# Kernel optimization log

Measured on AMD Instinct MI355X. Metric: run time of the kernel, lower is better.

The kernel has to match this reference:

```python
import jax, jax.numpy as jnp
import numpy as np

C = 64  # chunk size (hardcoded in DeltaCorrection.forward)


def setup_inputs() -> dict:
    key = jax.random.key(0)
    ks = jax.random.split(key, 6)
    B, H, N, d = 4, 16, 4096, 64
    q = jax.random.normal(ks[0], (B, H, N, d), jnp.float32)
    k = jax.random.normal(ks[1], (B, H, N, d), jnp.float32)
    v = jax.random.normal(ks[2], (B, H, N, d), jnp.float32)
    # gate projections: Linear(d, 1). Use small random weights so gates vary per token.
    w_decay = jax.random.normal(ks[3], (d, 1), jnp.float32) * 0.1
    b_decay = jnp.full((1,), -2.0, jnp.float32)
    w_write = jax.random.normal(ks[4], (d, 1), jnp.float32) * 0.1
    b_write = jnp.full((1,), -1.0, jnp.float32)
    out_scale = jnp.full((1,), 0.01, jnp.float32)
    return {"q": q, "k": k, "v": v, "w_decay": w_decay, "b_decay": b_decay,
            "w_write": w_write, "b_write": b_write, "out_scale": out_scale}


def _delta_correction(q, k, v, w_decay, b_decay, w_write, b_write, out_scale):
    B, H, N, d = q.shape
    assert N % C == 0  # pad branch is a no-op for our shapes
    beta = jax.nn.sigmoid(k @ w_write + b_write)   # (B,H,N,1) write strength
    alpha = jax.nn.sigmoid(k @ w_decay + b_decay)  # (B,H,N,1) decay
    k_norm = k / jnp.maximum(jnp.linalg.norm(k, axis=-1, keepdims=True), 1e-12)

    n_chunks = N // C
    q_c = q.reshape(B, H, n_chunks, C, d)
    k_c = k_norm.reshape(B, H, n_chunks, C, d)
    v_c = v.reshape(B, H, n_chunks, C, d)
    b_c = beta.reshape(B, H, n_chunks, C, 1)
    a_c = alpha.reshape(B, H, n_chunks, C, 1)

    # intra-chunk causal linear attention, scaled by per-key beta
    scores = jnp.einsum('bhnid,bhnjd->bhnij', q_c, k_c)      # (B,H,n,C,C)
    causal = jnp.tril(jnp.ones((C, C), q.dtype))
    scores = scores * causal * jnp.swapaxes(b_c, -1, -2)
    intra = jnp.einsum('bhnij,bhnjd->bhnid', scores, v_c)     # (B,H,n,C,d)

    # inter-chunk: sequential (d,d) state propagation via scan
    chunk_decay = jnp.mean(a_c, axis=3) ** C                  # (B,H,n,1)
    kv_all = jnp.einsum('bhnci,bhncj->bhnij', b_c * v_c, k_c) # (B,H,n,d,d)

    def step(S, inp):
        qc, kvc, dec = inp  # (B,H,C,d), (B,H,d,d), (B,H,1)
        inter = jnp.einsum('bhij,bhcj->bhci', S, qc)
        S = dec[..., None] * S + kvc
        return S, inter

    xs = (jnp.moveaxis(q_c, 2, 0), jnp.moveaxis(kv_all, 2, 0),
          jnp.moveaxis(chunk_decay, 2, 0))
    S0 = jnp.zeros((B, H, d, d), q.dtype)
    _, inter = jax.lax.scan(step, S0, xs)                     # (n,B,H,C,d)
    inter = jnp.moveaxis(inter, 0, 2)                         # (B,H,n,C,d)

    corrections = (intra + inter).reshape(B, H, N, d)
    return corrections * out_scale[0]


def reference(q, k, v, w_decay, b_decay, w_write, b_write, out_scale):
    return _delta_correction(q, k, v, w_decay, b_decay, w_write, b_write, out_scale)
```

## Files before the change

kernel.cpp:

```cpp
#include <hip/hip_runtime.h>
#include <math.h>


#define NCH 64
#define NBH 64

typedef __attribute__((ext_vector_type(8))) short bf16x8;
typedef __attribute__((ext_vector_type(4))) float f32x4;
typedef unsigned short ushort_t;

#define MFMA(a, b, c) __builtin_amdgcn_mfma_f32_16x16x32_bf16(a, b, c, 0, 0, 0)

__device__ __forceinline__ float sigf(float x) { return 1.0f / (1.0f + expf(-x)); }

__device__ __forceinline__ int swb(int row, int col) {
  return ((row << 7) + (col << 1)) ^ ((row & 7) << 4);
}

__device__ __forceinline__ void split1(float x, ushort_t& h, ushort_t& l) {
  unsigned xb = __float_as_uint(x);
  h = (ushort_t)(xb >> 16);
  float hf = __uint_as_float(xb & 0xFFFF0000u);
  float lf = x - hf;
  l = (ushort_t)(__float_as_uint(lf) >> 16);
}

__device__ __forceinline__ void st_split4(char* bh, char* bl, int row, int col, float4 v) {
  ushort_t h0, h1, h2, h3, l0, l1, l2, l3;
  split1(v.x, h0, l0); split1(v.y, h1, l1); split1(v.z, h2, l2); split1(v.w, h3, l3);
  uint2 hp, lp;
  hp.x = (unsigned)h0 | ((unsigned)h1 << 16); hp.y = (unsigned)h2 | ((unsigned)h3 << 16);
  lp.x = (unsigned)l0 | ((unsigned)l1 << 16); lp.y = (unsigned)l2 | ((unsigned)l3 << 16);
  int o = swb(row, col);
  *(uint2*)(bh + o) = hp;
  *(uint2*)(bl + o) = lp;
}

__device__ __forceinline__ bf16x8 ldfrag(const char* base, int mrow, int kk, int lane) {
  int r = mrow + (lane & 15);
  int c = kk + ((lane >> 4) << 3);
  return *(const bf16x8*)(base + swb(r, c));
}

__global__ __launch_bounds__(256) void k1_kvdecay(
    const float* __restrict__ kg, const float* __restrict__ vg,
    const float* __restrict__ w_decay, const float* __restrict__ b_decay,
    const float* __restrict__ w_write, const float* __restrict__ b_write,
    float* __restrict__ ws_kv, float* __restrict__ ws_decay) {
  __shared__ uint4 smraw[3072];
  __shared__ float abuf[64];
  char* sm = (char*)smraw;
  char* KT_H = sm;
  char* KT_L = sm + 8192;
  char* VT_H = sm + 16384;
  char* VT_L = sm + 24576;
  float* obuf = (float*)(sm + 32768);

  const int tid = threadIdx.x;
  const int lane = tid & 63, wv = tid >> 6;
  const int bh = blockIdx.x >> 6, cid = blockIdx.x & 63;
  const size_t gbase = (size_t)(bh * 4096 + cid * 64) * 64;

  {
    const int t = tid >> 2, g = tid & 3;
    const float* kp = kg + gbase + t * 64 + g * 16;
    const float* vp = vg + gbase + t * 64 + g * 16;
    float4 kr[4], vr[4];
#pragma unroll
    for (int u = 0; u < 4; ++u) { kr[u] = *(const float4*)(kp + 4 * u); vr[u] = *(const float4*)(vp + 4 * u); }
    float n2 = 0.f, dw = 0.f, da = 0.f;
#pragma unroll
    for (int u = 0; u < 4; ++u) {
      const float* wwp = w_write + g * 16 + 4 * u;
      const float* wdp = w_decay + g * 16 + 4 * u;
      float4 k4 = kr[u];
      n2 = fmaf(k4.x, k4.x, fmaf(k4.y, k4.y, fmaf(k4.z, k4.z, fmaf(k4.w, k4.w, n2))));
      dw = fmaf(k4.x, wwp[0], fmaf(k4.y, wwp[1], fmaf(k4.z, wwp[2], fmaf(k4.w, wwp[3], dw))));
      da = fmaf(k4.x, wdp[0], fmaf(k4.y, wdp[1], fmaf(k4.z, wdp[2], fmaf(k4.w, wdp[3], da))));
    }
    n2 += __shfl_xor(n2, 1, 64); n2 += __shfl_xor(n2, 2, 64);
    dw += __shfl_xor(dw, 1, 64); dw += __shfl_xor(dw, 2, 64);
    da += __shfl_xor(da, 1, 64); da += __shfl_xor(da, 2, 64);
    float beta  = sigf(dw + b_write[0]);
    float alpha = sigf(da + b_decay[0]);
    float fold  = beta / fmaxf(sqrtf(n2), 1e-12f);
    if (g == 0) abuf[t] = alpha;
#pragma unroll
    for (int u = 0; u < 4; ++u) {
      float kf[4] = {kr[u].x * fold, kr[u].y * fold, kr[u].z * fold, kr[u].w * fold};
      float vf[4] = {vr[u].x, vr[u].y, vr[u].z, vr[u].w};
#pragma unroll
      for (int e = 0; e < 4; ++e) {
        int row = g * 16 + 4 * u + e;
        ushort_t h, l;
        int o = swb(row, t);
        split1(kf[e], h, l);
        *(ushort_t*)(KT_H + o) = h; *(ushort_t*)(KT_L + o) = l;
        split1(vf[e], h, l);
        *(ushort_t*)(VT_H + o) = h; *(ushort_t*)(VT_L + o) = l;
      }
    }
  }
  __syncthreads();

  if (tid < 64) {
    float a = abuf[tid];
    for (int off = 32; off; off >>= 1) a += __shfl_down(a, off, 64);
    if (tid == 0) {
      float m = a * (1.0f / 64.0f);
      float p = m * m; p = p * p; p = p * p; p = p * p; p = p * p; p = p * p;
      ws_decay[bh * NCH + cid] = p;
    }
  }

  f32x4 z = {0.f, 0.f, 0.f, 0.f};
  f32x4 acc[4] = {z, z, z, z};
#pragma unroll
  for (int kk = 0; kk < 64; kk += 32) {
    bf16x8 ah = ldfrag(VT_H, wv * 16, kk, lane);
    bf16x8 al = ldfrag(VT_L, wv * 16, kk, lane);
#pragma unroll
    for (int jb = 0; jb < 4; ++jb) {
      bf16x8 bh_ = ldfrag(KT_H, jb * 16, kk, lane);
      bf16x8 bl_ = ldfrag(KT_L, jb * 16, kk, lane);
      acc[jb] = MFMA(ah, bh_, acc[jb]);
      acc[jb] = MFMA(ah, bl_, acc[jb]);
      acc[jb] = MFMA(al, bh_, acc[jb]);
    }
  }
#pragma unroll
  for (int jb = 0; jb < 4; ++jb) {
    int j = jb * 16 + (lane & 15);
    int i0 = wv * 16 + ((lane >> 4) << 2);
#pragma unroll
    for (int r = 0; r < 4; ++r) obuf[(i0 + r) * 64 + j] = acc[jb][r];
  }
  __syncthreads();
  float* kvout = ws_kv + (size_t)(bh * NCH + cid) * 4096;
#pragma unroll
  for (int rr = 0; rr < 4; ++rr) {
    int f = tid + 256 * rr;
    *(float4*)(kvout + f * 4) = *(const float4*)(obuf + f * 4);
  }
}

__global__ __launch_bounds__(256) void k2_scan(float* __restrict__ ws_kv,
                                               const float* __restrict__ ws_decay) {
  const int bh = blockIdx.x >> 2;
  const int pos = (blockIdx.x & 3) * 256 + threadIdx.x;
  float4* base = (float4*)ws_kv + (size_t)bh * 65536 + pos;
  const float* dec = ws_decay + bh * NCH;
  float4 S = make_float4(0.f, 0.f, 0.f, 0.f);
#pragma unroll
  for (int gq = 0; gq < 8; ++gq) {
    float4 buf[8];
#pragma unroll
    for (int j = 0; j < 8; ++j) buf[j] = base[(size_t)(gq * 8 + j) * 1024];
#pragma unroll
    for (int j = 0; j < 8; ++j) {
      int c = gq * 8 + j;
      float dcy = dec[c];
      base[(size_t)c * 1024] = S;
      S.x = fmaf(dcy, S.x, buf[j].x);
      S.y = fmaf(dcy, S.y, buf[j].y);
      S.z = fmaf(dcy, S.z, buf[j].z);
      S.w = fmaf(dcy, S.w, buf[j].w);
    }
  }
}

__global__ __launch_bounds__(256) void k3_out(
    const float* __restrict__ qg, const float* __restrict__ kg,
    const float* __restrict__ vg,
    const float* __restrict__ w_write, const float* __restrict__ b_write,
    const float* __restrict__ out_scale,
    const float* __restrict__ ws_kv, float* __restrict__ outg) {
  __shared__ uint4 smraw[4096];
  char* sm = (char*)smraw;
  char* QS_H = sm;             char* QS_L = sm + 8192;
  char* KS_H = sm + 16384;     char* KS_L = sm + 24576;
  char* VT_H = sm + 32768;     char* VT_L = sm + 40960;
  char* SS_H = sm + 49152;     char* SS_L = sm + 57344;
  char* PS_H = KS_H;           char* PS_L = KS_L;
  float* obuf = (float*)sm;

  const int tid = threadIdx.x;
  const int lane = tid & 63, wv = tid >> 6;
  const int bh = blockIdx.x >> 6, cid = blockIdx.x & 63;
  const size_t gbase = (size_t)(bh * 4096 + cid * 64) * 64;
  const float* Sg = ws_kv + (size_t)(bh * NCH + cid) * 4096;

#pragma unroll
  for (int rr = 0; rr < 4; ++rr) {
    int f = tid + 256 * rr;
    int row = f >> 4, c4 = (f & 15) * 4;
    float4 qq = *(const float4*)(qg + gbase + row * 64 + c4);
    st_split4(QS_H, QS_L, row, c4, qq);
    float4 sv = *(const float4*)(Sg + row * 64 + c4);
    st_split4(SS_H, SS_L, row, c4, sv);
    float4 vv = *(const float4*)(vg + gbase + row * 64 + c4);
    float vf[4] = {vv.x, vv.y, vv.z, vv.w};
#pragma unroll
    for (int e = 0; e < 4; ++e) {
      ushort_t h, l;
      split1(vf[e], h, l);
      int o = swb(c4 + e, row);
      *(ushort_t*)(VT_H + o) = h; *(ushort_t*)(VT_L + o) = l;
    }
  }
  {
    const int t = tid >> 2, g = tid & 3;
    const float* kp = kg + gbase + t * 64 + g * 16;
    float4 kr[4];
#pragma unroll
    for (int u = 0; u < 4; ++u) kr[u] = *(const float4*)(kp + 4 * u);
    float n2 = 0.f, dw = 0.f;
#pragma unroll
    for (int u = 0; u < 4; ++u) {
      const float* wwp = w_write + g * 16 + 4 * u;
      float4 k4 = kr[u];
      n2 = fmaf(k4.x, k4.x, fmaf(k4.y, k4.y, fmaf(k4.z, k4.z, fmaf(k4.w, k4.w, n2))));
      dw = fmaf(k4.x, wwp[0], fmaf(k4.y, wwp[1], fmaf(k4.z, wwp[2], fmaf(k4.w, wwp[3], dw))));
    }
    n2 += __shfl_xor(n2, 1, 64); n2 += __shfl_xor(n2, 2, 64);
    dw += __shfl_xor(dw, 1, 64); dw += __shfl_xor(dw, 2, 64);
    float beta = sigf(dw + b_write[0]);
    float fold = beta / fmaxf(sqrtf(n2), 1e-12f);
#pragma unroll
    for (int u = 0; u < 4; ++u) {
      float4 kf4 = make_float4(kr[u].x * fold, kr[u].y * fold, kr[u].z * fold, kr[u].w * fold);
      st_split4(KS_H, KS_L, t, g * 16 + 4 * u, kf4);
    }
  }
  __syncthreads();

  f32x4 z = {0.f, 0.f, 0.f, 0.f};
  f32x4 accs[4] = {z, z, z, z};
#pragma unroll
  for (int kk = 0; kk < 64; kk += 32) {
    bf16x8 ah = ldfrag(KS_H, wv * 16, kk, lane);
    bf16x8 al = ldfrag(KS_L, wv * 16, kk, lane);
#pragma unroll
    for (int nb = 0; nb < 4; ++nb) {
      bf16x8 bh_ = ldfrag(QS_H, nb * 16, kk, lane);
      bf16x8 bl_ = ldfrag(QS_L, nb * 16, kk, lane);
      accs[nb] = MFMA(ah, bh_, accs[nb]);
      accs[nb] = MFMA(ah, bl_, accs[nb]);
      accs[nb] = MFMA(al, bh_, accs[nb]);
    }
  }
  __syncthreads();

#pragma unroll
  for (int nb = 0; nb < 4; ++nb) {
    int tcol = nb * 16 + (lane & 15);
    int j0 = wv * 16 + ((lane >> 4) << 2);
    float x0 = (j0 + 0 <= tcol) ? accs[nb][0] : 0.f;
    float x1 = (j0 + 1 <= tcol) ? accs[nb][1] : 0.f;
    float x2 = (j0 + 2 <= tcol) ? accs[nb][2] : 0.f;
    float x3 = (j0 + 3 <= tcol) ? accs[nb][3] : 0.f;
    st_split4(PS_H, PS_L, tcol, j0, make_float4(x0, x1, x2, x3));
  }
  __syncthreads();

  f32x4 acco[4] = {z, z, z, z};
#pragma unroll
  for (int kk = 0; kk < 64; kk += 32) {
    bf16x8 ah = ldfrag(QS_H, wv * 16, kk, lane);
    bf16x8 al = ldfrag(QS_L, wv * 16, kk, lane);
#pragma unroll
    for (int ib = 0; ib < 4; ++ib) {
      bf16x8 bh_ = ldfrag(SS_H, ib * 16, kk, lane);
      bf16x8 bl_ = ldfrag(SS_L, ib * 16, kk, lane);
      acco[ib] = MFMA(ah, bh_, acco[ib]);
      acco[ib] = MFMA(ah, bl_, acco[ib]);
      acco[ib] = MFMA(al, bh_, acco[ib]);
    }
  }
#pragma unroll
  for (int kk = 0; kk < 64; kk += 32) {
    bf16x8 ah = ldfrag(PS_H, wv * 16, kk, lane);
    bf16x8 al = ldfrag(PS_L, wv * 16, kk, lane);
#pragma unroll
    for (int ib = 0; ib < 4; ++ib) {
      bf16x8 bh_ = ldfrag(VT_H, ib * 16, kk, lane);
      bf16x8 bl_ = ldfrag(VT_L, ib * 16, kk, lane);
      acco[ib] = MFMA(ah, bh_, acco[ib]);
      acco[ib] = MFMA(ah, bl_, acco[ib]);
      acco[ib] = MFMA(al, bh_, acco[ib]);
    }
  }
  __syncthreads();

  const float osc = out_scale[0];
#pragma unroll
  for (int ib = 0; ib < 4; ++ib) {
    int i = ib * 16 + (lane & 15);
    int t0 = wv * 16 + ((lane >> 4) << 2);
#pragma unroll
    for (int r = 0; r < 4; ++r) obuf[(t0 + r) * 64 + i] = acco[ib][r] * osc;
  }
  __syncthreads();
#pragma unroll
  for (int rr = 0; rr < 4; ++rr) {
    int f = tid + 256 * rr;
    *(float4*)(outg + gbase + f * 4) = *(const float4*)(obuf + f * 4);
  }
}

extern "C" void kernel_launch(void* const* d_in, const int* in_sizes, int n_in,
                              void* d_out, int out_size, void* d_ws, size_t ws_size,
                              hipStream_t stream) {
  const float* q         = (const float*)d_in[0];
  const float* k         = (const float*)d_in[1];
  const float* v         = (const float*)d_in[2];
  const float* w_decay   = (const float*)d_in[3];
  const float* b_decay   = (const float*)d_in[4];
  const float* w_write   = (const float*)d_in[5];
  const float* b_write   = (const float*)d_in[6];
  const float* out_scale = (const float*)d_in[7];
  float* out = (float*)d_out;

  float* ws_kv    = (float*)d_ws;
  float* ws_decay = ws_kv + (size_t)NBH * NCH * 4096;

  k1_kvdecay<<<dim3(NBH * NCH), dim3(256), 0, stream>>>(
      k, v, w_decay, b_decay, w_write, b_write, ws_kv, ws_decay);
  k2_scan<<<dim3(256), dim3(256), 0, stream>>>(ws_kv, ws_decay);
  k3_out<<<dim3(NBH * NCH), dim3(256), 0, stream>>>(
      q, k, v, w_write, b_write, out_scale, ws_kv, out);
}
```

Measured before the change: 282.7 us.

## Fuse chunk KV, scan and output into one persistent sequential kernel

Replaces the three-kernel pipeline (per-chunk KV outer products, global scan over the workspace, output kernel) with one kernel. Each block owns one (batch, head) and a 16-column slice of the state, keeps the state in registers, and walks all 64 chunks in order. It double-buffers the global loads of the next chunk and splits the work between Q-side and K-side waves. This removes the large workspace round-trip and two launches. In exchange only 256 blocks run, each with a long serial chain of chunks and several barriers per chunk, and the intra-chunk score computation is redone four times per head.

After: 590.1 us. 109% more time.

```diff
diff --git a/kernel.cpp b/kernel.cpp
--- a/kernel.cpp
+++ b/kernel.cpp
@@ -1,15 +1,13 @@
 #include <hip/hip_runtime.h>
 #include <math.h>
 
-
-#define NCH 64
-#define NBH 64
 
 typedef __attribute__((ext_vector_type(8))) short bf16x8;
 typedef __attribute__((ext_vector_type(4))) float f32x4;
 typedef unsigned short ushort_t;
 
 #define MFMA(a, b, c) __builtin_amdgcn_mfma_f32_16x16x32_bf16(a, b, c, 0, 0, 0)
+#define GETC(v, u) ((u) == 0 ? (v).x : ((u) == 1 ? (v).y : ((u) == 2 ? (v).z : (v).w)))
 
 __device__ __forceinline__ float sigf(float x) { return 1.0f / (1.0f + expf(-x)); }
 
@@ -42,269 +40,208 @@
   return *(const bf16x8*)(base + swb(r, c));
 }
 
-__global__ __launch_bounds__(256) void k1_kvdecay(
-    const float* __restrict__ kg, const float* __restrict__ vg,
+__global__ __launch_bounds__(512) void fused_delta(
+    const float* __restrict__ qg, const float* __restrict__ kg,
+    const float* __restrict__ vg,
     const float* __restrict__ w_decay, const float* __restrict__ b_decay,
     const float* __restrict__ w_write, const float* __restrict__ b_write,
-    float* __restrict__ ws_kv, float* __restrict__ ws_decay) {
-  __shared__ uint4 smraw[3072];
-  __shared__ float abuf[64];
-  char* sm = (char*)smraw;
-  char* KT_H = sm;
-  char* KT_L = sm + 8192;
-  char* VT_H = sm + 16384;
-  char* VT_L = sm + 24576;
-  float* obuf = (float*)(sm + 32768);
-
-  const int tid = threadIdx.x;
-  const int lane = tid & 63, wv = tid >> 6;
-  const int bh = blockIdx.x >> 6, cid = blockIdx.x & 63;
-  const size_t gbase = (size_t)(bh * 4096 + cid * 64) * 64;
-
-  {
-    const int t = tid >> 2, g = tid & 3;
-    const float* kp = kg + gbase + t * 64 + g * 16;
-    const float* vp = vg + gbase + t * 64 + g * 16;
-    float4 kr[4], vr[4];
-#pragma unroll
-    for (int u = 0; u < 4; ++u) { kr[u] = *(const float4*)(kp + 4 * u); vr[u] = *(const float4*)(vp + 4 * u); }
-    float n2 = 0.f, dw = 0.f, da = 0.f;
-#pragma unroll
-    for (int u = 0; u < 4; ++u) {
-      const float* wwp = w_write + g * 16 + 4 * u;
-      const float* wdp = w_decay + g * 16 + 4 * u;
-      float4 k4 = kr[u];
-      n2 = fmaf(k4.x, k4.x, fmaf(k4.y, k4.y, fmaf(k4.z, k4.z, fmaf(k4.w, k4.w, n2))));
-      dw = fmaf(k4.x, wwp[0], fmaf(k4.y, wwp[1], fmaf(k4.z, wwp[2], fmaf(k4.w, wwp[3], dw))));
-      da = fmaf(k4.x, wdp[0], fmaf(k4.y, wdp[1], fmaf(k4.z, wdp[2], fmaf(k4.w, wdp[3], da))));
-    }
-    n2 += __shfl_xor(n2, 1, 64); n2 += __shfl_xor(n2, 2, 64);
-    dw += __shfl_xor(dw, 1, 64); dw += __shfl_xor(dw, 2, 64);
-    da += __shfl_xor(da, 1, 64); da += __shfl_xor(da, 2, 64);
-    float beta  = sigf(dw + b_write[0]);
-    float alpha = sigf(da + b_decay[0]);
-    float fold  = beta / fmaxf(sqrtf(n2), 1e-12f);
-    if (g == 0) abuf[t] = alpha;
-#pragma unroll
-    for (int u = 0; u < 4; ++u) {
-      float kf[4] = {kr[u].x * fold, kr[u].y * fold, kr[u].z * fold, kr[u].w * fold};
-      float vf[4] = {vr[u].x, vr[u].y, vr[u].z, vr[u].w};
-#pragma unroll
-      for (int e = 0; e < 4; ++e) {
-        int row = g * 16 + 4 * u + e;
-        ushort_t h, l;
-        int o = swb(row, t);
-        split1(kf[e], h, l);
-        *(ushort_t*)(KT_H + o) = h; *(ushort_t*)(KT_L + o) = l;
-        split1(vf[e], h, l);
-        *(ushort_t*)(VT_H + o) = h; *(ushort_t*)(VT_L + o) = l;
-      }
-    }
-  }
-  __syncthreads();
-
-  if (tid < 64) {
-    float a = abuf[tid];
-    for (int off = 32; off; off >>= 1) a += __shfl_down(a, off, 64);
-    if (tid == 0) {
-      float m = a * (1.0f / 64.0f);
-      float p = m * m; p = p * p; p = p * p; p = p * p; p = p * p; p = p * p;
-      ws_decay[bh * NCH + cid] = p;
-    }
-  }
-
-  f32x4 z = {0.f, 0.f, 0.f, 0.f};
-  f32x4 acc[4] = {z, z, z, z};
-#pragma unroll
-  for (int kk = 0; kk < 64; kk += 32) {
-    bf16x8 ah = ldfrag(VT_H, wv * 16, kk, lane);
-    bf16x8 al = ldfrag(VT_L, wv * 16, kk, lane);
-#pragma unroll
-    for (int jb = 0; jb < 4; ++jb) {
-      bf16x8 bh_ = ldfrag(KT_H, jb * 16, kk, lane);
-      bf16x8 bl_ = ldfrag(KT_L, jb * 16, kk, lane);
-      acc[jb] = MFMA(ah, bh_, acc[jb]);
-      acc[jb] = MFMA(ah, bl_, acc[jb]);
-      acc[jb] = MFMA(al, bh_, acc[jb]);
-    }
-  }
-#pragma unroll
-  for (int jb = 0; jb < 4; ++jb) {
-    int j = jb * 16 + (lane & 15);
-    int i0 = wv * 16 + ((lane >> 4) << 2);
-#pragma unroll
-    for (int r = 0; r < 4; ++r) obuf[(i0 + r) * 64 + j] = acc[jb][r];
-  }
-  __syncthreads();
-  float* kvout = ws_kv + (size_t)(bh * NCH + cid) * 4096;
-#pragma unroll
-  for (int rr = 0; rr < 4; ++rr) {
-    int f = tid + 256 * rr;
-    *(float4*)(kvout + f * 4) = *(const float4*)(obuf + f * 4);
-  }
-}
-
-__global__ __launch_bounds__(256) void k2_scan(float* __restrict__ ws_kv,
-                                               const float* __restrict__ ws_decay) {
-  const int bh = blockIdx.x >> 2;
-  const int pos = (blockIdx.x & 3) * 256 + threadIdx.x;
-  float4* base = (float4*)ws_kv + (size_t)bh * 65536 + pos;
-  const float* dec = ws_decay + bh * NCH;
-  float4 S = make_float4(0.f, 0.f, 0.f, 0.f);
-#pragma unroll
-  for (int gq = 0; gq < 8; ++gq) {
-    float4 buf[8];
-#pragma unroll
-    for (int j = 0; j < 8; ++j) buf[j] = base[(size_t)(gq * 8 + j) * 1024];
-#pragma unroll
-    for (int j = 0; j < 8; ++j) {
-      int c = gq * 8 + j;
-      float dcy = dec[c];
-      base[(size_t)c * 1024] = S;
-      S.x = fmaf(dcy, S.x, buf[j].x);
-      S.y = fmaf(dcy, S.y, buf[j].y);
-      S.z = fmaf(dcy, S.z, buf[j].z);
-      S.w = fmaf(dcy, S.w, buf[j].w);
-    }
-  }
-}
-
-__global__ __launch_bounds__(256) void k3_out(
-    const float* __restrict__ qg, const float* __restrict__ kg,
-    const float* __restrict__ vg,
-    const float* __restrict__ w_write, const float* __restrict__ b_write,
-    const float* __restrict__ out_scale,
-    const float* __restrict__ ws_kv, float* __restrict__ outg) {
-  __shared__ uint4 smraw[4096];
+    const float* __restrict__ out_scale, float* __restrict__ outg) {
+  __shared__ uint4 smraw[3601];
   char* sm = (char*)smraw;
   char* QS_H = sm;             char* QS_L = sm + 8192;
   char* KS_H = sm + 16384;     char* KS_L = sm + 24576;
-  char* VT_H = sm + 32768;     char* VT_L = sm + 40960;
-  char* SS_H = sm + 49152;     char* SS_L = sm + 57344;
-  char* PS_H = KS_H;           char* PS_L = KS_L;
-  float* obuf = (float*)sm;
-
-  const int tid = threadIdx.x;
-  const int lane = tid & 63, wv = tid >> 6;
-  const int bh = blockIdx.x >> 6, cid = blockIdx.x & 63;
-  const size_t gbase = (size_t)(bh * 4096 + cid * 64) * 64;
-  const float* Sg = ws_kv + (size_t)(bh * NCH + cid) * 4096;
-
-#pragma unroll
-  for (int rr = 0; rr < 4; ++rr) {
-    int f = tid + 256 * rr;
-    int row = f >> 4, c4 = (f & 15) * 4;
-    float4 qq = *(const float4*)(qg + gbase + row * 64 + c4);
-    st_split4(QS_H, QS_L, row, c4, qq);
-    float4 sv = *(const float4*)(Sg + row * 64 + c4);
-    st_split4(SS_H, SS_L, row, c4, sv);
-    float4 vv = *(const float4*)(vg + gbase + row * 64 + c4);
-    float vf[4] = {vv.x, vv.y, vv.z, vv.w};
-#pragma unroll
-    for (int e = 0; e < 4; ++e) {
-      ushort_t h, l;
-      split1(vf[e], h, l);
-      int o = swb(c4 + e, row);
-      *(ushort_t*)(VT_H + o) = h; *(ushort_t*)(VT_L + o) = l;
-    }
+  char* KT_H = sm + 32768;     char* KT_L = sm + 40960;
+  char* VT_H = sm + 49152;     char* VT_L = sm + 51200;
+  char* SL_H = sm + 53248;     char* SL_L = sm + 55296;
+  float* abuf = (float*)(sm + 57344);
+  float* decp = (float*)(sm + 57600);
+
+  const int tid = threadIdx.x, lane = tid & 63, wv = tid >> 6;
+  const int bh = blockIdx.x >> 2, qd = blockIdx.x & 3, ibase = qd * 16;
+  const size_t sbase = (size_t)bh * 262144;
+
+  const float bwr = b_write[0], bdc = b_decay[0], osc = out_scale[0];
+
+  const bool isK = (tid >= 256);
+  const int tk = tid - 256, ktq = tk >> 4, kc4 = tk & 15;
+  const int qrow = tid >> 2, qc16 = (tid & 3) << 4;
+  const int vtq = tid >> 2, vmq = tid & 3;
+  float4 ww4 = make_float4(0.f, 0.f, 0.f, 0.f), wd4 = ww4;
+  if (isK) {
+    ww4 = *(const float4*)(w_write + kc4 * 4);
+    wd4 = *(const float4*)(w_decay + kc4 * 4);
   }
-  {
-    const int t = tid >> 2, g = tid & 3;
-    const float* kp = kg + gbase + t * 64 + g * 16;
-    float4 kr[4];
-#pragma unroll
-    for (int u = 0; u < 4; ++u) kr[u] = *(const float4*)(kp + 4 * u);
-    float n2 = 0.f, dw = 0.f;
-#pragma unroll
-    for (int u = 0; u < 4; ++u) {
-      const float* wwp = w_write + g * 16 + 4 * u;
-      float4 k4 = kr[u];
-      n2 = fmaf(k4.x, k4.x, fmaf(k4.y, k4.y, fmaf(k4.z, k4.z, fmaf(k4.w, k4.w, n2))));
-      dw = fmaf(k4.x, wwp[0], fmaf(k4.y, wwp[1], fmaf(k4.z, wwp[2], fmaf(k4.w, wwp[3], dw))));
-    }
-    n2 += __shfl_xor(n2, 1, 64); n2 += __shfl_xor(n2, 2, 64);
-    dw += __shfl_xor(dw, 1, 64); dw += __shfl_xor(dw, 2, 64);
-    float beta = sigf(dw + b_write[0]);
-    float fold = beta / fmaxf(sqrtf(n2), 1e-12f);
-#pragma unroll
-    for (int u = 0; u < 4; ++u) {
-      float4 kf4 = make_float4(kr[u].x * fold, kr[u].y * fold, kr[u].z * fold, kr[u].w * fold);
-      st_split4(KS_H, KS_L, t, g * 16 + 4 * u, kf4);
-    }
-  }
-  __syncthreads();
-
-  f32x4 z = {0.f, 0.f, 0.f, 0.f};
-  f32x4 accs[4] = {z, z, z, z};
-#pragma unroll
-  for (int kk = 0; kk < 64; kk += 32) {
-    bf16x8 ah = ldfrag(KS_H, wv * 16, kk, lane);
-    bf16x8 al = ldfrag(KS_L, wv * 16, kk, lane);
-#pragma unroll
-    for (int nb = 0; nb < 4; ++nb) {
-      bf16x8 bh_ = ldfrag(QS_H, nb * 16, kk, lane);
-      bf16x8 bl_ = ldfrag(QS_L, nb * 16, kk, lane);
-      accs[nb] = MFMA(ah, bh_, accs[nb]);
-      accs[nb] = MFMA(ah, bl_, accs[nb]);
-      accs[nb] = MFMA(al, bh_, accs[nb]);
-    }
-  }
-  __syncthreads();
-
-#pragma unroll
-  for (int nb = 0; nb < 4; ++nb) {
-    int tcol = nb * 16 + (lane & 15);
-    int j0 = wv * 16 + ((lane >> 4) << 2);
-    float x0 = (j0 + 0 <= tcol) ? accs[nb][0] : 0.f;
-    float x1 = (j0 + 1 <= tcol) ? accs[nb][1] : 0.f;
-    float x2 = (j0 + 2 <= tcol) ? accs[nb][2] : 0.f;
-    float x3 = (j0 + 3 <= tcol) ? accs[nb][3] : 0.f;
-    st_split4(PS_H, PS_L, tcol, j0, make_float4(x0, x1, x2, x3));
-  }
-  __syncthreads();
-
-  f32x4 acco[4] = {z, z, z, z};
-#pragma unroll
-  for (int kk = 0; kk < 64; kk += 32) {
-    bf16x8 ah = ldfrag(QS_H, wv * 16, kk, lane);
-    bf16x8 al = ldfrag(QS_L, wv * 16, kk, lane);
-#pragma unroll
-    for (int ib = 0; ib < 4; ++ib) {
-      bf16x8 bh_ = ldfrag(SS_H, ib * 16, kk, lane);
-      bf16x8 bl_ = ldfrag(SS_L, ib * 16, kk, lane);
-      acco[ib] = MFMA(ah, bh_, acco[ib]);
-      acco[ib] = MFMA(ah, bl_, acco[ib]);
-      acco[ib] = MFMA(al, bh_, acco[ib]);
-    }
-  }
-#pragma unroll
-  for (int kk = 0; kk < 64; kk += 32) {
-    bf16x8 ah = ldfrag(PS_H, wv * 16, kk, lane);
-    bf16x8 al = ldfrag(PS_L, wv * 16, kk, lane);
-#pragma unroll
-    for (int ib = 0; ib < 4; ++ib) {
-      bf16x8 bh_ = ldfrag(VT_H, ib * 16, kk, lane);
-      bf16x8 bl_ = ldfrag(VT_L, ib * 16, kk, lane);
-      acco[ib] = MFMA(ah, bh_, acco[ib]);
-      acco[ib] = MFMA(ah, bl_, acco[ib]);
-      acco[ib] = MFMA(al, bh_, acco[ib]);
-    }
-  }
-  __syncthreads();
-
-  const float osc = out_scale[0];
-#pragma unroll
-  for (int ib = 0; ib < 4; ++ib) {
-    int i = ib * 16 + (lane & 15);
-    int t0 = wv * 16 + ((lane >> 4) << 2);
-#pragma unroll
-    for (int r = 0; r < 4; ++r) obuf[(t0 + r) * 64 + i] = acco[ib][r] * osc;
-  }
-  __syncthreads();
-#pragma unroll
-  for (int rr = 0; rr < 4; ++rr) {
-    int f = tid + 256 * rr;
-    *(float4*)(outg + gbase + f * 4) = *(const float4*)(obuf + f * 4);
+
+  float4 qr0[4], qr1[4], vr0[4], vr1[4], kr0[4], kr1[4];
+
+  auto LOADC = [&](float4 (&qr)[4], float4 (&vr)[4], float4 (&kr)[4], int c) {
+    const size_t cb = sbase + (size_t)c * 4096;
+    if (!isK) {
+      const float* qp = qg + cb + qrow * 64 + qc16;
+#pragma unroll
+      for (int u = 0; u < 4; ++u) qr[u] = *(const float4*)(qp + 4 * u);
+      if (tid < 64) {
+#pragma unroll
+        for (int e = 0; e < 4; ++e)
+          vr[e] = *(const float4*)(vg + cb + (vtq * 4 + e) * 64 + ibase + vmq * 4);
+      }
+    } else {
+#pragma unroll
+      for (int e = 0; e < 4; ++e)
+        kr[e] = *(const float4*)(kg + cb + (ktq * 4 + e) * 64 + kc4 * 4);
+    }
+  };
+
+  f32x4 S = {0.f, 0.f, 0.f, 0.f};
+  const f32x4 z = {0.f, 0.f, 0.f, 0.f};
+
+  auto BODY = [&](float4 (&qr)[4], float4 (&vr)[4], float4 (&kr)[4], int c, int cnext) {
+    if (!isK) {
+#pragma unroll
+      for (int u = 0; u < 4; ++u) st_split4(QS_H, QS_L, qrow, qc16 + 4 * u, qr[u]);
+      if (tid < 64) {
+#pragma unroll
+        for (int mm = 0; mm < 4; ++mm) {
+          float4 tv = make_float4(GETC(vr[0], mm), GETC(vr[1], mm),
+                                  GETC(vr[2], mm), GETC(vr[3], mm));
+          st_split4(VT_H, VT_L, vmq * 4 + mm, vtq * 4, tv);
+        }
+      }
+    } else {
+      float n2[4], dw[4], da[4];
+#pragma unroll
+      for (int e = 0; e < 4; ++e) {
+        float4 k4 = kr[e];
+        n2[e] = k4.x * k4.x + k4.y * k4.y + k4.z * k4.z + k4.w * k4.w;
+        dw[e] = k4.x * ww4.x + k4.y * ww4.y + k4.z * ww4.z + k4.w * ww4.w;
+        da[e] = k4.x * wd4.x + k4.y * wd4.y + k4.z * wd4.z + k4.w * wd4.w;
+      }
+#pragma unroll
+      for (int m = 1; m < 16; m <<= 1) {
+#pragma unroll
+        for (int e = 0; e < 4; ++e) {
+          n2[e] += __shfl_xor(n2[e], m, 64);
+          dw[e] += __shfl_xor(dw[e], m, 64);
+          da[e] += __shfl_xor(da[e], m, 64);
+        }
+      }
+      float4 kf[4];
+#pragma unroll
+      for (int e = 0; e < 4; ++e) {
+        float beta  = sigf(dw[e] + bwr);
+        float alpha = sigf(da[e] + bdc);
+        float fold  = beta / fmaxf(sqrtf(n2[e]), 1e-12f);
+        if (kc4 == 0) abuf[ktq * 4 + e] = alpha;
+        kf[e] = make_float4(kr[e].x * fold, kr[e].y * fold, kr[e].z * fold, kr[e].w * fold);
+        st_split4(KS_H, KS_L, ktq * 4 + e, kc4 * 4, kf[e]);
+      }
+#pragma unroll
+      for (int m = 0; m < 4; ++m) {
+        float4 tv = make_float4(GETC(kf[0], m), GETC(kf[1], m),
+                                GETC(kf[2], m), GETC(kf[3], m));
+        st_split4(KT_H, KT_L, kc4 * 4 + m, ktq * 4, tv);
+      }
+    }
+    LOADC(qr, vr, kr, cnext);
+    __syncthreads();
+
+    f32x4 sc[2] = {z, z};
+    __builtin_amdgcn_s_setprio(1);
+#pragma unroll
+    for (int s = 0; s < 2; ++s) {
+      int tt = wv * 2 + s, jb = tt >> 2, tb = tt & 3;
+#pragma unroll
+      for (int kk = 0; kk < 64; kk += 32) {
+        bf16x8 ah = ldfrag(KS_H, jb * 16, kk, lane), al = ldfrag(KS_L, jb * 16, kk, lane);
+        bf16x8 bh_ = ldfrag(QS_H, tb * 16, kk, lane), bl_ = ldfrag(QS_L, tb * 16, kk, lane);
+        sc[s] = MFMA(ah, bh_, sc[s]);
+        sc[s] = MFMA(ah, bl_, sc[s]);
+        sc[s] = MFMA(al, bh_, sc[s]);
+      }
+    }
+    __builtin_amdgcn_s_setprio(0);
+    if (wv == 4) {
+      float a = abuf[lane];
+#pragma unroll
+      for (int off = 32; off; off >>= 1) a += __shfl_down(a, off, 64);
+      if (lane == 0) {
+        float m_ = a * (1.0f / 64.0f);
+        float p = m_ * m_; p = p * p; p = p * p; p = p * p; p = p * p; p = p * p;
+        *decp = p;
+      }
+    }
+    __syncthreads();
+
+#pragma unroll
+    for (int s = 0; s < 2; ++s) {
+      int tt = wv * 2 + s, jb = tt >> 2, tb = tt & 3;
+      int tcol = tb * 16 + (lane & 15), j0 = jb * 16 + ((lane >> 4) << 2);
+      float x0 = (j0 + 0 <= tcol) ? sc[s][0] : 0.f;
+      float x1 = (j0 + 1 <= tcol) ? sc[s][1] : 0.f;
+      float x2 = (j0 + 2 <= tcol) ? sc[s][2] : 0.f;
+      float x3 = (j0 + 3 <= tcol) ? sc[s][3] : 0.f;
+      st_split4(KS_H, KS_L, tcol, j0, make_float4(x0, x1, x2, x3));
+    }
+    f32x4 kvacc = z;
+    if (wv < 4) {
+      int j = wv * 16 + (lane & 15), i0 = (lane >> 4) << 2;
+#pragma unroll
+      for (int r = 0; r < 4; ++r) {
+        ushort_t h, l;
+        split1(S[r], h, l);
+        int o = swb(i0 + r, j);
+        *(ushort_t*)(SL_H + o) = h;
+        *(ushort_t*)(SL_L + o) = l;
+      }
+      __builtin_amdgcn_s_setprio(1);
+#pragma unroll
+      for (int kk = 0; kk < 64; kk += 32) {
+        bf16x8 ah = ldfrag(VT_H, 0, kk, lane), al = ldfrag(VT_L, 0, kk, lane);
+        bf16x8 bh_ = ldfrag(KT_H, wv * 16, kk, lane), bl_ = ldfrag(KT_L, wv * 16, kk, lane);
+        kvacc = MFMA(ah, bh_, kvacc);
+        kvacc = MFMA(ah, bl_, kvacc);
+        kvacc = MFMA(al, bh_, kvacc);
+      }
+      __builtin_amdgcn_s_setprio(0);
+    }
+    __syncthreads();
+
+    if (wv >= 4) {
+      int tb = wv - 4;
+      f32x4 acc = z;
+      __builtin_amdgcn_s_setprio(1);
+#pragma unroll
+      for (int kk = 0; kk < 64; kk += 32) {
+        bf16x8 ah = ldfrag(SL_H, 0, kk, lane), al = ldfrag(SL_L, 0, kk, lane);
+        bf16x8 bh_ = ldfrag(QS_H, tb * 16, kk, lane), bl_ = ldfrag(QS_L, tb * 16, kk, lane);
+        acc = MFMA(ah, bh_, acc);
+        acc = MFMA(ah, bl_, acc);
+        acc = MFMA(al, bh_, acc);
+        bf16x8 ch = ldfrag(VT_H, 0, kk, lane), cl = ldfrag(VT_L, 0, kk, lane);
+        bf16x8 dh = ldfrag(KS_H, tb * 16, kk, lane), dl = ldfrag(KS_L, tb * 16, kk, lane);
+        acc = MFMA(ch, dh, acc);
+        acc = MFMA(ch, dl, acc);
+        acc = MFMA(cl, dh, acc);
+      }
+      __builtin_amdgcn_s_setprio(0);
+      int t = tb * 16 + (lane & 15), i0 = (lane >> 4) << 2;
+      float4 o = make_float4(acc[0] * osc, acc[1] * osc, acc[2] * osc, acc[3] * osc);
+      *(float4*)(outg + sbase + (size_t)c * 4096 + t * 64 + ibase + i0) = o;
+    } else {
+      float dcy = *decp;
+      S[0] = fmaf(dcy, S[0], kvacc[0]);
+      S[1] = fmaf(dcy, S[1], kvacc[1]);
+      S[2] = fmaf(dcy, S[2], kvacc[2]);
+      S[3] = fmaf(dcy, S[3], kvacc[3]);
+    }
+    __syncthreads();
+  };
+
+  LOADC(qr0, vr0, kr0, 0);
+  LOADC(qr1, vr1, kr1, 1);
+  for (int c = 0; c < 64; c += 2) {
+    BODY(qr0, vr0, kr0, c,     (c + 2 < 64) ? c + 2 : 63);
+    BODY(qr1, vr1, kr1, c + 1, (c + 3 < 64) ? c + 3 : 63);
   }
 }
 
@@ -321,12 +258,6 @@
   const float* out_scale = (const float*)d_in[7];
   float* out = (float*)d_out;
 
-  float* ws_kv    = (float*)d_ws;
-  float* ws_decay = ws_kv + (size_t)NBH * NCH * 4096;
-
-  k1_kvdecay<<<dim3(NBH * NCH), dim3(256), 0, stream>>>(
-      k, v, w_decay, b_decay, w_write, b_write, ws_kv, ws_decay);
-  k2_scan<<<dim3(256), dim3(256), 0, stream>>>(ws_kv, ws_decay);
-  k3_out<<<dim3(NBH * NCH), dim3(256), 0, stream>>>(
-      q, k, v, w_write, b_write, out_scale, ws_kv, out);
-}
+  fused_delta<<<dim3(256), dim3(512), 0, stream>>>(
+      q, k, v, w_decay, b_decay, w_write, b_write, out_scale, out);
+}
```

## Cut LDS staging in chunk kernels, load S fragments directly, raise occupancy

Applied to the files above, without the earlier changes.

k1 now writes the kv accumulator tiles straight to global memory instead of staging them through shared memory. k3 loads the state matrix S into registers in MFMA fragment order and splits it to bf16 hi/lo in registers, which removes the SS shared buffers. It also writes output directly from the accumulators, transposes V in registers before the swizzled LDS store, and interleaves the two output GEMMs. Shared memory per block shrinks and launch bounds request 4 and 3 blocks per CU. The cost is less-coalesced scalar global stores and higher register pressure.

Measured after the change: 288.7 us. 2.1% more time.

```diff
diff --git a/kernel.cpp b/kernel.cpp
--- a/kernel.cpp
+++ b/kernel.cpp
@@ -10,6 +10,7 @@
 typedef unsigned short ushort_t;
 
 #define MFMA(a, b, c) __builtin_amdgcn_mfma_f32_16x16x32_bf16(a, b, c, 0, 0, 0)
+#define GETC(v, u) ((u) == 0 ? (v).x : ((u) == 1 ? (v).y : ((u) == 2 ? (v).z : (v).w)))
 
 __device__ __forceinline__ float sigf(float x) { return 1.0f / (1.0f + expf(-x)); }
 
@@ -42,19 +43,30 @@
   return *(const bf16x8*)(base + swb(r, c));
 }
 
-__global__ __launch_bounds__(256) void k1_kvdecay(
+__device__ __forceinline__ void split8(float4 a, float4 b, bf16x8& h, bf16x8& l) {
+  float x[8] = {a.x, a.y, a.z, a.w, b.x, b.y, b.z, b.w};
+  bf16x8 hh, ll;
+#pragma unroll
+  for (int i = 0; i < 8; ++i) {
+    ushort_t hi, lo;
+    split1(x[i], hi, lo);
+    hh[i] = (short)hi; ll[i] = (short)lo;
+  }
+  h = hh; l = ll;
+}
+
+__global__ __launch_bounds__(256, 4) void k1_kvdecay(
     const float* __restrict__ kg, const float* __restrict__ vg,
     const float* __restrict__ w_decay, const float* __restrict__ b_decay,
     const float* __restrict__ w_write, const float* __restrict__ b_write,
     float* __restrict__ ws_kv, float* __restrict__ ws_decay) {
-  __shared__ uint4 smraw[3072];
-  __shared__ float abuf[64];
+  __shared__ uint4 smraw[2064];
   char* sm = (char*)smraw;
   char* KT_H = sm;
   char* KT_L = sm + 8192;
   char* VT_H = sm + 16384;
   char* VT_L = sm + 24576;
-  float* obuf = (float*)(sm + 32768);
+  float* abuf = (float*)(sm + 32768);
 
   const int tid = threadIdx.x;
   const int lane = tid & 63, wv = tid >> 6;
@@ -128,19 +140,15 @@
       acc[jb] = MFMA(al, bh_, acc[jb]);
     }
   }
-#pragma unroll
-  for (int jb = 0; jb < 4; ++jb) {
-    int j = jb * 16 + (lane & 15);
+  float* kvout = ws_kv + (size_t)(bh * NCH + cid) * 4096;
+  {
     int i0 = wv * 16 + ((lane >> 4) << 2);
 #pragma unroll
-    for (int r = 0; r < 4; ++r) obuf[(i0 + r) * 64 + j] = acc[jb][r];
-  }
-  __syncthreads();
-  float* kvout = ws_kv + (size_t)(bh * NCH + cid) * 4096;
-#pragma unroll
-  for (int rr = 0; rr < 4; ++rr) {
-    int f = tid + 256 * rr;
-    *(float4*)(kvout + f * 4) = *(const float4*)(obuf + f * 4);
+    for (int jb = 0; jb < 4; ++jb) {
+      int j = jb * 16 + (lane & 15);
+#pragma unroll
+      for (int r = 0; r < 4; ++r) kvout[(i0 + r) * 64 + j] = acc[jb][r];
+    }
   }
 }
 
@@ -169,20 +177,18 @@
   }
 }
 
-__global__ __launch_bounds__(256) void k3_out(
+__global__ __launch_bounds__(256, 3) void k3_out(
     const float* __restrict__ qg, const float* __restrict__ kg,
     const float* __restrict__ vg,
     const float* __restrict__ w_write, const float* __restrict__ b_write,
     const float* __restrict__ out_scale,
     const float* __restrict__ ws_kv, float* __restrict__ outg) {
-  __shared__ uint4 smraw[4096];
+  __shared__ uint4 smraw[3072];
   char* sm = (char*)smraw;
   char* QS_H = sm;             char* QS_L = sm + 8192;
   char* KS_H = sm + 16384;     char* KS_L = sm + 24576;
   char* VT_H = sm + 32768;     char* VT_L = sm + 40960;
-  char* SS_H = sm + 49152;     char* SS_L = sm + 57344;
   char* PS_H = KS_H;           char* PS_L = KS_L;
-  float* obuf = (float*)sm;
 
   const int tid = threadIdx.x;
   const int lane = tid & 63, wv = tid >> 6;
@@ -196,16 +202,17 @@
     int row = f >> 4, c4 = (f & 15) * 4;
     float4 qq = *(const float4*)(qg + gbase + row * 64 + c4);
     st_split4(QS_H, QS_L, row, c4, qq);
-    float4 sv = *(const float4*)(Sg + row * 64 + c4);
-    st_split4(SS_H, SS_L, row, c4, sv);
-    float4 vv = *(const float4*)(vg + gbase + row * 64 + c4);
-    float vf[4] = {vv.x, vv.y, vv.z, vv.w};
-#pragma unroll
-    for (int e = 0; e < 4; ++e) {
-      ushort_t h, l;
-      split1(vf[e], h, l);
-      int o = swb(c4 + e, row);
-      *(ushort_t*)(VT_H + o) = h; *(ushort_t*)(VT_L + o) = l;
+  }
+  {
+    const int rq = tid & 15, cq = tid >> 4;
+    float4 vv[4];
+#pragma unroll
+    for (int e = 0; e < 4; ++e)
+      vv[e] = *(const float4*)(vg + gbase + (4 * rq + e) * 64 + 4 * cq);
+#pragma unroll
+    for (int m = 0; m < 4; ++m) {
+      float4 tv = make_float4(GETC(vv[0], m), GETC(vv[1], m), GETC(vv[2], m), GETC(vv[3], m));
+      st_split4(VT_H, VT_L, 4 * cq + m, 4 * rq, tv);
     }
   }
   {
@@ -250,6 +257,20 @@
     }
   }
   __syncthreads();
+
+  float4 sraw[16];
+  {
+    const int l15 = lane & 15, g8 = (lane >> 4) << 3;
+#pragma unroll
+    for (int ib = 0; ib < 4; ++ib) {
+#pragma unroll
+      for (int k2 = 0; k2 < 2; ++k2) {
+        const float* p = Sg + (ib * 16 + l15) * 64 + k2 * 32 + g8;
+        sraw[ib * 4 + k2 * 2 + 0] = *(const float4*)(p);
+        sraw[ib * 4 + k2 * 2 + 1] = *(const float4*)(p + 4);
+      }
+    }
+  }
 
 #pragma unroll
   for (int nb = 0; nb < 4; ++nb) {
@@ -265,46 +286,37 @@
 
   f32x4 acco[4] = {z, z, z, z};
 #pragma unroll
-  for (int kk = 0; kk < 64; kk += 32) {
-    bf16x8 ah = ldfrag(QS_H, wv * 16, kk, lane);
-    bf16x8 al = ldfrag(QS_L, wv * 16, kk, lane);
+  for (int k2 = 0; k2 < 2; ++k2) {
+    const int kk = k2 * 32;
+    bf16x8 qh = ldfrag(QS_H, wv * 16, kk, lane);
+    bf16x8 ql = ldfrag(QS_L, wv * 16, kk, lane);
+    bf16x8 ph = ldfrag(PS_H, wv * 16, kk, lane);
+    bf16x8 pl = ldfrag(PS_L, wv * 16, kk, lane);
 #pragma unroll
     for (int ib = 0; ib < 4; ++ib) {
-      bf16x8 bh_ = ldfrag(SS_H, ib * 16, kk, lane);
-      bf16x8 bl_ = ldfrag(SS_L, ib * 16, kk, lane);
-      acco[ib] = MFMA(ah, bh_, acco[ib]);
-      acco[ib] = MFMA(ah, bl_, acco[ib]);
-      acco[ib] = MFMA(al, bh_, acco[ib]);
-    }
-  }
-#pragma unroll
-  for (int kk = 0; kk < 64; kk += 32) {
-    bf16x8 ah = ldfrag(PS_H, wv * 16, kk, lane);
-    bf16x8 al = ldfrag(PS_L, wv * 16, kk, lane);
+      bf16x8 sh, sl;
+      split8(sraw[ib * 4 + k2 * 2 + 0], sraw[ib * 4 + k2 * 2 + 1], sh, sl);
+      acco[ib] = MFMA(qh, sh, acco[ib]);
+      acco[ib] = MFMA(qh, sl, acco[ib]);
+      acco[ib] = MFMA(ql, sh, acco[ib]);
+      bf16x8 vh = ldfrag(VT_H, ib * 16, kk, lane);
+      bf16x8 vl = ldfrag(VT_L, ib * 16, kk, lane);
+      acco[ib] = MFMA(ph, vh, acco[ib]);
+      acco[ib] = MFMA(ph, vl, acco[ib]);
+      acco[ib] = MFMA(pl, vh, acco[ib]);
+    }
+  }
+
+  const float osc = out_scale[0];
+  {
+    int t0 = wv * 16 + ((lane >> 4) << 2);
+    int l15 = lane & 15;
 #pragma unroll
     for (int ib = 0; ib < 4; ++ib) {
-      bf16x8 bh_ = ldfrag(VT_H, ib * 16, kk, lane);
-      bf16x8 bl_ = ldfrag(VT_L, ib * 16, kk, lane);
-      acco[ib] = MFMA(ah, bh_, acco[ib]);
-      acco[ib] = MFMA(ah, bl_, acco[ib]);
-      acco[ib] = MFMA(al, bh_, acco[ib]);
-    }
-  }
-  __syncthreads();
-
-  const float osc = out_scale[0];
-#pragma unroll
-  for (int ib = 0; ib < 4; ++ib) {
-    int i = ib * 16 + (lane & 15);
-    int t0 = wv * 16 + ((lane >> 4) << 2);
-#pragma unroll
-    for (int r = 0; r < 4; ++r) obuf[(t0 + r) * 64 + i] = acco[ib][r] * osc;
-  }
-  __syncthreads();
-#pragma unroll
-  for (int rr = 0; rr < 4; ++rr) {
-    int f = tid + 256 * rr;
-    *(float4*)(outg + gbase + f * 4) = *(const float4*)(obuf + f * 4);
+#pragma unroll
+      for (int r = 0; r < 4; ++r)
+        outg[gbase + (t0 + r) * 64 + ib * 16 + l15] = acco[ib][r] * osc;
+    }
   }
 }
 
```
